# Kernel optimization log

Hardware: AMD Instinct MI355X
Metric: run time of the kernel (lower is better)

The kernel has to match this reference:

```python
import jax, jax.numpy as jnp
import numpy as np

N_NODES = 1048576
N_EDGES = 16777216
N_GRAPHS = 64
K_HOPS = 4


def setup_inputs() -> dict:
    key = jax.random.key(0)
    k1, k2, k3 = jax.random.split(key, 3)
    x = jax.random.normal(k1, (N_NODES, 1), dtype=jnp.float32)
    edge_index = jax.random.randint(k2, (2, N_EDGES), 0, N_NODES, dtype=jnp.int64)
    W = jax.random.normal(k3, (1, 1), dtype=jnp.float32)
    b = jnp.zeros((1,), dtype=jnp.float32)
    return {"x": x, "edge_index": edge_index, "W": W, "b": b, "num_graphs": N_GRAPHS}


def _sgconv(x, edge_index, W, b, k):
    # PyG SGConv: x <- (D^-1/2 (A + I) D^-1/2)^k x, then linear.
    n = x.shape[0]
    loops = jnp.arange(n, dtype=edge_index.dtype)
    row = jnp.concatenate([edge_index[0], loops])  # source nodes
    col = jnp.concatenate([edge_index[1], loops])  # target nodes
    ones = jnp.ones(row.shape[0], dtype=x.dtype)
    deg = jax.ops.segment_sum(ones, col, num_segments=n)  # in-degree incl. self loop
    dinv = jnp.where(deg > 0, jax.lax.rsqrt(deg), 0.0)
    norm = dinv[row] * dinv[col]  # [E+N]
    for _ in range(k):
        x = jax.ops.segment_sum(norm[:, None] * x[row], col, num_segments=n)
    return x @ W.T + b


def reference(x, edge_index, W, b, num_graphs):
    h = _sgconv(x, edge_index, W, b, K_HOPS)  # [N, 1]
    n = h.shape[0]
    # tensor_split into num_graphs equal chunks (N divisible by num_graphs), mean each
    out = h.reshape(num_graphs, n // num_graphs, 1).mean(axis=1)  # [B, 1]
    return out
```

## Files before the change

kernel.cpp:

```cpp
#include <hip/hip_runtime.h>
#include <stdint.h>

#define N_NODES  (1u << 20)
#define N_EDGES  (1u << 24)
#define N_GRAPHS 64
#define CHUNK    (N_NODES / N_GRAPHS)
#define K_HOPS   4

#define NBUCKET  1024
#define CPB      1024
#define CAP      18432

#define NBLK_SS  512
#define TB_SS    1024
#define EPT      32
#define EPB_SS   (TB_SS * EPT)

typedef uint32_t u32x4 __attribute__((ext_vector_type(4)));
typedef unsigned long long u64x2 __attribute__((ext_vector_type(2)));

__device__ __forceinline__ u32x4 nt_load_u32x4(const uint32_t* p) {
    return __builtin_nontemporal_load((const u32x4*)p);
}
__device__ __forceinline__ u64x2 nt_load_u64x2(const unsigned long long* p) {
    return __builtin_nontemporal_load((const u64x2*)p);
}

__global__ __launch_bounds__(TB_SS, 4)
void scatter_sort_kernel(const void* __restrict__ ei,
                         int* __restrict__ cursor, uint32_t* __restrict__ packed) {
    __shared__ uint32_t sorted[EPB_SS];
    __shared__ int h[NBUCKET];
    __shared__ int o[NBUCKET];
    __shared__ int ostart[NBUCKET];
    __shared__ int gbase[NBUCKET];
    __shared__ int s_is64;
    int blk = blockIdx.x, tid = threadIdx.x;
    h[tid] = 0;
    size_t base = (size_t)blk * EPB_SS;

    if (tid < 64) {
        size_t widx = 2 * base + 2 * (size_t)tid * 512 + 1;
        int nz = (((const uint32_t*)ei)[widx] != 0u);
        unsigned long long m = __ballot(nz);
        if (tid == 0) s_is64 = (m == 0ull) ? 1 : 0;
    }
    __syncthreads();
    int is64 = s_is64;
    uint32_t c_[EPT];

    if (is64) {
        const unsigned long long* cp = (const unsigned long long*)ei + N_EDGES + base;
        #pragma unroll
        for (int it = 0; it < EPT / 4; ++it) {
            size_t i = (size_t)it * (TB_SS * 4) + (size_t)tid * 4;
            u64x2 a = nt_load_u64x2(cp + i);
            u64x2 b2 = nt_load_u64x2(cp + i + 2);
            c_[it * 4 + 0] = (uint32_t)a.x;  c_[it * 4 + 1] = (uint32_t)a.y;
            c_[it * 4 + 2] = (uint32_t)b2.x; c_[it * 4 + 3] = (uint32_t)b2.y;
            atomicAdd(&h[c_[it * 4 + 0] >> 10], 1);
            atomicAdd(&h[c_[it * 4 + 1] >> 10], 1);
            atomicAdd(&h[c_[it * 4 + 2] >> 10], 1);
            atomicAdd(&h[c_[it * 4 + 3] >> 10], 1);
        }
    } else {
        const uint32_t* cp = (const uint32_t*)ei + N_EDGES + base;
        #pragma unroll
        for (int it = 0; it < EPT / 4; ++it) {
            size_t i = (size_t)it * (TB_SS * 4) + (size_t)tid * 4;
            u32x4 a = nt_load_u32x4(cp + i);
            c_[it * 4 + 0] = a.x; c_[it * 4 + 1] = a.y;
            c_[it * 4 + 2] = a.z; c_[it * 4 + 3] = a.w;
            atomicAdd(&h[a.x >> 10], 1);
            atomicAdd(&h[a.y >> 10], 1);
            atomicAdd(&h[a.z >> 10], 1);
            atomicAdd(&h[a.w >> 10], 1);
        }
    }
    __syncthreads();

    if (tid < 64) {
        int b16 = tid * 16;
        int s = 0;
        #pragma unroll
        for (int j = 0; j < 16; ++j) s += h[b16 + j];
        int v = s;
        #pragma unroll
        for (int off = 1; off < 64; off <<= 1) {
            int up = __shfl_up(v, off, 64);
            if (tid >= off) v += up;
        }
        int run = v - s;
        #pragma unroll
        for (int j = 0; j < 16; ++j) {
            o[b16 + j] = run;
            ostart[b16 + j] = run;
            run += h[b16 + j];
        }
    }
    __syncthreads();

    gbase[tid] = atomicAdd(&cursor[tid], h[tid]);

    if (is64) {
        const unsigned long long* rp = (const unsigned long long*)ei + base;
        #pragma unroll
        for (int it = 0; it < EPT / 4; ++it) {
            size_t i = (size_t)it * (TB_SS * 4) + (size_t)tid * 4;
            u64x2 a = nt_load_u64x2(rp + i);
            u64x2 b2 = nt_load_u64x2(rp + i + 2);
            uint32_t r0 = (uint32_t)a.x, r1 = (uint32_t)a.y;
            uint32_t r2 = (uint32_t)b2.x, r3 = (uint32_t)b2.y;
            { uint32_t c = c_[it * 4 + 0]; int pos = atomicAdd(&o[c >> 10], 1); sorted[pos] = (r0 << 10) | (c & 1023u); }
            { uint32_t c = c_[it * 4 + 1]; int pos = atomicAdd(&o[c >> 10], 1); sorted[pos] = (r1 << 10) | (c & 1023u); }
            { uint32_t c = c_[it * 4 + 2]; int pos = atomicAdd(&o[c >> 10], 1); sorted[pos] = (r2 << 10) | (c & 1023u); }
            { uint32_t c = c_[it * 4 + 3]; int pos = atomicAdd(&o[c >> 10], 1); sorted[pos] = (r3 << 10) | (c & 1023u); }
        }
    } else {
        const uint32_t* rp = (const uint32_t*)ei + base;
        #pragma unroll
        for (int it = 0; it < EPT / 4; ++it) {
            size_t i = (size_t)it * (TB_SS * 4) + (size_t)tid * 4;
            u32x4 a = nt_load_u32x4(rp + i);
            { uint32_t c = c_[it * 4 + 0]; int pos = atomicAdd(&o[c >> 10], 1); sorted[pos] = (a.x << 10) | (c & 1023u); }
            { uint32_t c = c_[it * 4 + 1]; int pos = atomicAdd(&o[c >> 10], 1); sorted[pos] = (a.y << 10) | (c & 1023u); }
            { uint32_t c = c_[it * 4 + 2]; int pos = atomicAdd(&o[c >> 10], 1); sorted[pos] = (a.z << 10) | (c & 1023u); }
            { uint32_t c = c_[it * 4 + 3]; int pos = atomicAdd(&o[c >> 10], 1); sorted[pos] = (a.w << 10) | (c & 1023u); }
        }
    }
    __syncthreads();

    int wave = tid >> 6, lane = tid & 63;
    for (int k = 0; k < NBUCKET / 16; ++k) {
        int b = wave * (NBUCKET / 16) + k;
        int st = ostart[b];
        int len = o[b] - st;
        int gb = gbase[b];
        if (gb + len > CAP) len = CAP - gb > 0 ? CAP - gb : 0;
        uint32_t* dst = packed + (size_t)b * CAP + gb;
        for (int j = lane; j < len; j += 64)
            dst[j] = sorted[st + j];
    }
}

__global__ __launch_bounds__(512)
void degdinv_kernel(const uint32_t* __restrict__ packed, const int* __restrict__ cursor,
                    const float* __restrict__ x,
                    float* __restrict__ dinv, float* __restrict__ z) {
    __shared__ int h[CPB];
    int b = blockIdx.x, tid = threadIdx.x;
    for (int l = tid; l < CPB; l += 512) h[l] = 0;
    __syncthreads();
    int cnt = cursor[b]; if (cnt > CAP) cnt = CAP;
    const uint32_t* seg = packed + (size_t)b * CAP;
    int nq = cnt >> 2;
    int g = tid;
    for (; g + 1536 < nq; g += 2048) {
        u32x4 q[4];
        q[0] = nt_load_u32x4(seg + 4 * (size_t)g);
        q[1] = nt_load_u32x4(seg + 4 * ((size_t)g + 512));
        q[2] = nt_load_u32x4(seg + 4 * ((size_t)g + 1024));
        q[3] = nt_load_u32x4(seg + 4 * ((size_t)g + 1536));
        #pragma unroll
        for (int j = 0; j < 4; ++j) {
            atomicAdd(&h[q[j].x & 1023u], 1);
            atomicAdd(&h[q[j].y & 1023u], 1);
            atomicAdd(&h[q[j].z & 1023u], 1);
            atomicAdd(&h[q[j].w & 1023u], 1);
        }
    }
    for (; g < nq; g += 512) {
        u32x4 v = nt_load_u32x4(seg + 4 * (size_t)g);
        atomicAdd(&h[v.x & 1023u], 1);
        atomicAdd(&h[v.y & 1023u], 1);
        atomicAdd(&h[v.z & 1023u], 1);
        atomicAdd(&h[v.w & 1023u], 1);
    }
    int t = (nq << 2) + tid;
    if (t < cnt) atomicAdd(&h[seg[t] & 1023u], 1);
    __syncthreads();
    for (int l = tid; l < CPB; l += 512) {
        int v = b * CPB + l;
        float d = (float)(1.0 / sqrt((double)(h[l] + 1)));
        dinv[v] = d;
        z[v] = d * x[v];
    }
}

__global__ __launch_bounds__(512)
void hop_kernel(const uint32_t* __restrict__ packed, const int* __restrict__ cursor,
                const float* __restrict__ z, const float* __restrict__ dinv,
                float* __restrict__ out) {
    __shared__ float facc[CPB];
    int b = blockIdx.x, tid = threadIdx.x;
    for (int l = tid; l < CPB; l += 512) facc[l] = 0.0f;
    __syncthreads();
    int cnt = cursor[b]; if (cnt > CAP) cnt = CAP;
    const uint32_t* seg = packed + (size_t)b * CAP;
    int nq = cnt >> 2;
    int g = tid;
    for (; g + 1536 < nq; g += 2048) {
        u32x4 q[4];
        q[0] = nt_load_u32x4(seg + 4 * (size_t)g);
        q[1] = nt_load_u32x4(seg + 4 * ((size_t)g + 512));
        q[2] = nt_load_u32x4(seg + 4 * ((size_t)g + 1024));
        q[3] = nt_load_u32x4(seg + 4 * ((size_t)g + 1536));
        float zv[16];
        #pragma unroll
        for (int j = 0; j < 4; ++j) {
            zv[4 * j + 0] = z[q[j].x >> 10];
            zv[4 * j + 1] = z[q[j].y >> 10];
            zv[4 * j + 2] = z[q[j].z >> 10];
            zv[4 * j + 3] = z[q[j].w >> 10];
        }
        #pragma unroll
        for (int j = 0; j < 4; ++j) {
            atomicAdd(&facc[q[j].x & 1023u], zv[4 * j + 0]);
            atomicAdd(&facc[q[j].y & 1023u], zv[4 * j + 1]);
            atomicAdd(&facc[q[j].z & 1023u], zv[4 * j + 2]);
            atomicAdd(&facc[q[j].w & 1023u], zv[4 * j + 3]);
        }
    }
    for (; g < nq; g += 512) {
        u32x4 v = nt_load_u32x4(seg + 4 * (size_t)g);
        float z0 = z[v.x >> 10];
        float z1 = z[v.y >> 10];
        float z2 = z[v.z >> 10];
        float z3 = z[v.w >> 10];
        atomicAdd(&facc[v.x & 1023u], z0);
        atomicAdd(&facc[v.y & 1023u], z1);
        atomicAdd(&facc[v.z & 1023u], z2);
        atomicAdd(&facc[v.w & 1023u], z3);
    }
    int t = (nq << 2) + tid;
    if (t < cnt) { uint32_t p = seg[t]; atomicAdd(&facc[p & 1023u], z[p >> 10]); }
    __syncthreads();
    for (int l = tid; l < CPB; l += 512) {
        int v = b * CPB + l;
        float tt = z[v] + facc[l];
        float d = dinv[v];
        out[v] = d * d * tt;
    }
}

__global__ __launch_bounds__(512)
void hop_final_kernel(const uint32_t* __restrict__ packed, const int* __restrict__ cursor,
                      const float* __restrict__ z, const float* __restrict__ dinv,
                      float* __restrict__ gsum) {
    __shared__ float facc[CPB];
    __shared__ double sdata[8];
    int b = blockIdx.x, tid = threadIdx.x;
    for (int l = tid; l < CPB; l += 512) facc[l] = 0.0f;
    __syncthreads();
    int cnt = cursor[b]; if (cnt > CAP) cnt = CAP;
    const uint32_t* seg = packed + (size_t)b * CAP;
    int nq = cnt >> 2;
    int g = tid;
    for (; g + 1536 < nq; g += 2048) {
        u32x4 q[4];
        q[0] = nt_load_u32x4(seg + 4 * (size_t)g);
        q[1] = nt_load_u32x4(seg + 4 * ((size_t)g + 512));
        q[2] = nt_load_u32x4(seg + 4 * ((size_t)g + 1024));
        q[3] = nt_load_u32x4(seg + 4 * ((size_t)g + 1536));
        float zv[16];
        #pragma unroll
        for (int j = 0; j < 4; ++j) {
            zv[4 * j + 0] = z[q[j].x >> 10];
            zv[4 * j + 1] = z[q[j].y >> 10];
            zv[4 * j + 2] = z[q[j].z >> 10];
            zv[4 * j + 3] = z[q[j].w >> 10];
        }
        #pragma unroll
        for (int j = 0; j < 4; ++j) {
            atomicAdd(&facc[q[j].x & 1023u], zv[4 * j + 0]);
            atomicAdd(&facc[q[j].y & 1023u], zv[4 * j + 1]);
            atomicAdd(&facc[q[j].z & 1023u], zv[4 * j + 2]);
            atomicAdd(&facc[q[j].w & 1023u], zv[4 * j + 3]);
        }
    }
    for (; g < nq; g += 512) {
        u32x4 v = nt_load_u32x4(seg + 4 * (size_t)g);
        float z0 = z[v.x >> 10];
        float z1 = z[v.y >> 10];
        float z2 = z[v.z >> 10];
        float z3 = z[v.w >> 10];
        atomicAdd(&facc[v.x & 1023u], z0);
        atomicAdd(&facc[v.y & 1023u], z1);
        atomicAdd(&facc[v.z & 1023u], z2);
        atomicAdd(&facc[v.w & 1023u], z3);
    }
    int t = (nq << 2) + tid;
    if (t < cnt) { uint32_t p = seg[t]; atomicAdd(&facc[p & 1023u], z[p >> 10]); }
    __syncthreads();
    double s = 0.0;
    for (int l = tid; l < CPB; l += 512) {
        int v = b * CPB + l;
        s += (double)(dinv[v] * (z[v] + facc[l]));
    }
    #pragma unroll
    for (int off = 32; off > 0; off >>= 1) s += __shfl_down(s, off, 64);
    int wave = tid >> 6, lane = tid & 63;
    if (lane == 0) sdata[wave] = s;
    __syncthreads();
    if (tid == 0) {
        double tot = 0.0;
        #pragma unroll
        for (int w = 0; w < 8; ++w) tot += sdata[w];
        atomicAdd(&gsum[b >> 4], (float)tot);
    }
}

__global__ void finalize_kernel(const float* __restrict__ gsum,
                                const float* __restrict__ W, const float* __restrict__ b,
                                float* __restrict__ out) {
    int g = threadIdx.x;
    if (g < N_GRAPHS)
        out[g] = (float)((double)W[0] * ((double)gsum[g] / (double)CHUNK) + (double)b[0]);
}

__global__ void detect_kernel(const uint32_t* __restrict__ ei, int* __restrict__ flag) {
    __shared__ int any_nz;
    if (threadIdx.x == 0) any_nz = 0;
    __syncthreads();
    int nz = 0;
    for (int i = threadIdx.x; i < 32768; i += blockDim.x)
        nz |= (ei[2 * i + 1] != 0u);
    if (nz) atomicOr(&any_nz, 1);
    __syncthreads();
    if (threadIdx.x == 0) flag[0] = any_nz ? 0 : 1;
}

__global__ void zero_int_kernel(int* __restrict__ p) {
    int i = blockIdx.x * blockDim.x + threadIdx.x;
    p[i] = 0;
}

__device__ __forceinline__ int load_idx(const void* ei, int is64, size_t pos) {
    if (is64) return (int)((const unsigned long long*)ei)[pos];
    return ((const int*)ei)[pos];
}

__global__ void count_kernel(const void* __restrict__ ei, const int* __restrict__ flag,
                             int* __restrict__ deg) {
    int e = blockIdx.x * blockDim.x + threadIdx.x;
    int c = load_idx(ei, flag[0], (size_t)N_EDGES + (size_t)e);
    atomicAdd(&deg[c], 1);
}

__global__ void dinv_kernel(const int* __restrict__ deg, float* __restrict__ dinv) {
    int v = blockIdx.x * blockDim.x + threadIdx.x;
    dinv[v] = (float)(1.0 / sqrt((double)(deg[v] + 1)));
}

__global__ void prep_first2_kernel(const float* __restrict__ x, const float* __restrict__ dinv,
                                   float* __restrict__ z, float* __restrict__ acc) {
    int v = blockIdx.x * blockDim.x + threadIdx.x;
    float t = dinv[v] * x[v];
    z[v] = t;
    acc[v] = t;
}

__global__ void prep_mid_kernel(const float* __restrict__ dinv,
                                float* __restrict__ z, float* __restrict__ acc) {
    int v = blockIdx.x * blockDim.x + threadIdx.x;
    float d = dinv[v];
    float t = d * d * acc[v];
    z[v] = t;
    acc[v] = t;
}

__global__ void push_kernel(const void* __restrict__ ei, const int* __restrict__ flag,
                            const float* __restrict__ z, float* __restrict__ acc) {
    int e = blockIdx.x * blockDim.x + threadIdx.x;
    int is64 = flag[0];
    int r, c;
    if (is64) {
        const unsigned long long* p = (const unsigned long long*)ei;
        r = (int)p[e];
        c = (int)p[(size_t)N_EDGES + (size_t)e];
    } else {
        const int* p = (const int*)ei;
        r = p[e];
        c = p[(size_t)N_EDGES + (size_t)e];
    }
    __hip_atomic_fetch_add(&acc[c], z[r], __ATOMIC_RELAXED, __HIP_MEMORY_SCOPE_AGENT);
}

__global__ void final_scale_kernel(const float* __restrict__ dinv,
                                   const float* __restrict__ acc, float* __restrict__ xf) {
    int v = blockIdx.x * blockDim.x + threadIdx.x;
    xf[v] = dinv[v] * acc[v];
}

__global__ void pool_kernel(const float* __restrict__ xf,
                            const float* __restrict__ W, const float* __restrict__ b,
                            float* __restrict__ out) {
    __shared__ double sdata[256];
    int g = blockIdx.x;
    int base = g * CHUNK;
    double s = 0.0;
    for (int i = threadIdx.x; i < CHUNK; i += 256) s += (double)xf[base + i];
    sdata[threadIdx.x] = s;
    __syncthreads();
    for (int off = 128; off > 0; off >>= 1) {
        if (threadIdx.x < off) sdata[threadIdx.x] += sdata[threadIdx.x + off];
        __syncthreads();
    }
    if (threadIdx.x == 0)
        out[g] = (float)((double)W[0] * (sdata[0] / (double)CHUNK) + (double)b[0]);
}

extern "C" void kernel_launch(void* const* d_in, const int* in_sizes, int n_in,
                              void* d_out, int out_size, void* d_ws, size_t ws_size,
                              hipStream_t stream) {
    const float* x = (const float*)d_in[0];
    const void*  ei = d_in[1];
    const float* W = (const float*)d_in[2];
    const float* b = (const float*)d_in[3];
    float* out = (float*)d_out;

    char* ws = (char*)d_ws;
    const size_t MB4 = 4ull << 20;
    size_t off_cursor = 0;
    size_t off_gsum   = NBUCKET * 4;
    size_t off_dinv   = off_gsum + 256;
    size_t off_za     = off_dinv + MB4;
    size_t off_zb     = off_za + MB4;
    size_t off_packed = off_zb + MB4;
    size_t needed     = off_packed + (size_t)NBUCKET * CAP * 4;

    const int TB = 256;

    if (ws_size >= needed) {
        int*      cursor = (int*)(ws + off_cursor);
        float*    gsum   = (float*)(ws + off_gsum);
        float*    dinv   = (float*)(ws + off_dinv);
        float*    za     = (float*)(ws + off_za);
        float*    zb     = (float*)(ws + off_zb);
        uint32_t* packed = (uint32_t*)(ws + off_packed);

        hipMemsetAsync(ws, 0, NBUCKET * 4 + 256, stream);

        scatter_sort_kernel<<<NBLK_SS, TB_SS, 0, stream>>>(ei, cursor, packed);
        degdinv_kernel<<<NBUCKET, 512, 0, stream>>>(packed, cursor, x, dinv, za);

        hop_kernel<<<NBUCKET, 512, 0, stream>>>(packed, cursor, za, dinv, zb);
        hop_kernel<<<NBUCKET, 512, 0, stream>>>(packed, cursor, zb, dinv, za);
        hop_kernel<<<NBUCKET, 512, 0, stream>>>(packed, cursor, za, dinv, zb);
        hop_final_kernel<<<NBUCKET, 512, 0, stream>>>(packed, cursor, zb, dinv, gsum);

        finalize_kernel<<<1, 64, 0, stream>>>(gsum, W, b, out);
    } else {
        int*   flag = (int*)ws;
        float* dinv = (float*)(ws + 256);
        float* za   = (float*)(ws + 256 + MB4);
        float* zb   = (float*)(ws + 256 + 2 * MB4);
        int*   deg  = (int*)(ws + 256 + 3 * MB4);

        detect_kernel<<<1, TB, 0, stream>>>((const uint32_t*)ei, flag);
        zero_int_kernel<<<N_NODES / TB, TB, 0, stream>>>(deg);
        count_kernel<<<N_EDGES / TB, TB, 0, stream>>>(ei, flag, deg);
        dinv_kernel<<<N_NODES / TB, TB, 0, stream>>>(deg, dinv);

        prep_first2_kernel<<<N_NODES / TB, TB, 0, stream>>>(x, dinv, za, zb);
        push_kernel<<<N_EDGES / TB, TB, 0, stream>>>(ei, flag, za, zb);
        for (int h = 1; h < K_HOPS; ++h) {
            prep_mid_kernel<<<N_NODES / TB, TB, 0, stream>>>(dinv, za, zb);
            push_kernel<<<N_EDGES / TB, TB, 0, stream>>>(ei, flag, za, zb);
        }
        final_scale_kernel<<<N_NODES / TB, TB, 0, stream>>>(dinv, zb, za);
        pool_kernel<<<N_GRAPHS, TB, 0, stream>>>(za, W, b, out);
    }
}
```

Baseline: 625.2 us.

## Sort each bucket's packed edges by source range inside degree kernel

```diff
diff --git a/kernel.cpp b/kernel.cpp
--- a/kernel.cpp
+++ b/kernel.cpp
@@ -16,6 +16,9 @@
 #define EPT      32
 #define EPB_SS   (TB_SS * EPT)
 
+#define RBITS    9
+#define NRANGE   (1 << RBITS)
+
 typedef uint32_t u32x4 __attribute__((ext_vector_type(4)));
 typedef unsigned long long u64x2 __attribute__((ext_vector_type(2)));
 
@@ -24,6 +27,9 @@
 }
 __device__ __forceinline__ u64x2 nt_load_u64x2(const unsigned long long* p) {
     return __builtin_nontemporal_load((const u64x2*)p);
+}
+__device__ __forceinline__ void nt_store_u32x4(uint32_t* p, u32x4 v) {
+    __builtin_nontemporal_store(v, (u32x4*)p);
 }
 
 __global__ __launch_bounds__(TB_SS, 4)
@@ -143,42 +149,74 @@
     }
 }
 
-__global__ __launch_bounds__(512)
-void degdinv_kernel(const uint32_t* __restrict__ packed, const int* __restrict__ cursor,
-                    const float* __restrict__ x,
-                    float* __restrict__ dinv, float* __restrict__ z) {
+__global__ __launch_bounds__(512, 2)
+void degdinv_sort_kernel(uint32_t* __restrict__ packed, const int* __restrict__ cursor,
+                         const float* __restrict__ x,
+                         float* __restrict__ dinv, float* __restrict__ z) {
+    __shared__ uint32_t sbuf[CAP];
     __shared__ int h[CPB];
+    __shared__ int ro[NRANGE];
     int b = blockIdx.x, tid = threadIdx.x;
     for (int l = tid; l < CPB; l += 512) h[l] = 0;
+    for (int l = tid; l < NRANGE; l += 512) ro[l] = 0;
     __syncthreads();
     int cnt = cursor[b]; if (cnt > CAP) cnt = CAP;
-    const uint32_t* seg = packed + (size_t)b * CAP;
+    uint32_t* seg = packed + (size_t)b * CAP;
     int nq = cnt >> 2;
-    int g = tid;
-    for (; g + 1536 < nq; g += 2048) {
-        u32x4 q[4];
-        q[0] = nt_load_u32x4(seg + 4 * (size_t)g);
-        q[1] = nt_load_u32x4(seg + 4 * ((size_t)g + 512));
-        q[2] = nt_load_u32x4(seg + 4 * ((size_t)g + 1024));
-        q[3] = nt_load_u32x4(seg + 4 * ((size_t)g + 1536));
-        #pragma unroll
-        for (int j = 0; j < 4; ++j) {
-            atomicAdd(&h[q[j].x & 1023u], 1);
-            atomicAdd(&h[q[j].y & 1023u], 1);
-            atomicAdd(&h[q[j].z & 1023u], 1);
-            atomicAdd(&h[q[j].w & 1023u], 1);
-        }
-    }
-    for (; g < nq; g += 512) {
-        u32x4 v = nt_load_u32x4(seg + 4 * (size_t)g);
-        atomicAdd(&h[v.x & 1023u], 1);
-        atomicAdd(&h[v.y & 1023u], 1);
-        atomicAdd(&h[v.z & 1023u], 1);
-        atomicAdd(&h[v.w & 1023u], 1);
-    }
-    int t = (nq << 2) + tid;
-    if (t < cnt) atomicAdd(&h[seg[t] & 1023u], 1);
-    __syncthreads();
+
+    for (int g = tid; g < nq; g += 512) {
+        u32x4 v = *(const u32x4*)(seg + 4 * (size_t)g);
+        atomicAdd(&h[v.x & 1023u], 1); atomicAdd(&ro[v.x >> 21], 1);
+        atomicAdd(&h[v.y & 1023u], 1); atomicAdd(&ro[v.y >> 21], 1);
+        atomicAdd(&h[v.z & 1023u], 1); atomicAdd(&ro[v.z >> 21], 1);
+        atomicAdd(&h[v.w & 1023u], 1); atomicAdd(&ro[v.w >> 21], 1);
+    }
+    {
+        int t = (nq << 2) + tid;
+        if (t < cnt) { uint32_t p = seg[t]; atomicAdd(&h[p & 1023u], 1); atomicAdd(&ro[p >> 21], 1); }
+    }
+    __syncthreads();
+
+    if (tid < 64) {
+        int b8 = tid * 8;
+        int s = 0;
+        #pragma unroll
+        for (int j = 0; j < 8; ++j) s += ro[b8 + j];
+        int v = s;
+        #pragma unroll
+        for (int off = 1; off < 64; off <<= 1) {
+            int up = __shfl_up(v, off, 64);
+            if (tid >= off) v += up;
+        }
+        int run = v - s;
+        #pragma unroll
+        for (int j = 0; j < 8; ++j) { int c = ro[b8 + j]; ro[b8 + j] = run; run += c; }
+    }
+    __syncthreads();
+
+    for (int g = tid; g < nq; g += 512) {
+        u32x4 v = *(const u32x4*)(seg + 4 * (size_t)g);
+        { int p = atomicAdd(&ro[v.x >> 21], 1); sbuf[p] = v.x; }
+        { int p = atomicAdd(&ro[v.y >> 21], 1); sbuf[p] = v.y; }
+        { int p = atomicAdd(&ro[v.z >> 21], 1); sbuf[p] = v.z; }
+        { int p = atomicAdd(&ro[v.w >> 21], 1); sbuf[p] = v.w; }
+    }
+    {
+        int t = (nq << 2) + tid;
+        if (t < cnt) { uint32_t p = seg[t]; int q = atomicAdd(&ro[p >> 21], 1); sbuf[q] = p; }
+    }
+    __syncthreads();
+
+    for (int g = tid; g < nq; g += 512) {
+        u32x4 o4;
+        o4.x = sbuf[4 * g + 0]; o4.y = sbuf[4 * g + 1];
+        o4.z = sbuf[4 * g + 2]; o4.w = sbuf[4 * g + 3];
+        nt_store_u32x4(seg + 4 * (size_t)g, o4);
+    }
+    {
+        int t = (nq << 2) + tid;
+        if (t < cnt) __builtin_nontemporal_store(sbuf[t], seg + t);
+    }
     for (int l = tid; l < CPB; l += 512) {
         int v = b * CPB + l;
         float d = (float)(1.0 / sqrt((double)(h[l] + 1)));
@@ -442,7 +480,7 @@
         hipMemsetAsync(ws, 0, NBUCKET * 4 + 256, stream);
 
         scatter_sort_kernel<<<NBLK_SS, TB_SS, 0, stream>>>(ei, cursor, packed);
-        degdinv_kernel<<<NBUCKET, 512, 0, stream>>>(packed, cursor, x, dinv, za);
+        degdinv_sort_kernel<<<NBUCKET, 512, 0, stream>>>(packed, cursor, x, dinv, za);
 
         hop_kernel<<<NBUCKET, 512, 0, stream>>>(packed, cursor, za, dinv, zb);
         hop_kernel<<<NBUCKET, 512, 0, stream>>>(packed, cursor, zb, dinv, za);
```

Result: no change. 628.8 us (+0.6%).
